# Kernel optimization log

Hardware: AMD Instinct MI355X
Metric: run time of the kernel (lower is better)

The kernel has to match this reference:

```python
import jax, jax.numpy as jnp
import numpy as np

B, S, I, H = 64, 1024, 512, 512


def setup_inputs() -> dict:
    key = jax.random.key(0)
    ks = jax.random.split(key, 6)
    stdv = 1.0 / np.sqrt(H)
    return {
        "inputs": jax.random.normal(ks[0], (B, S, I), dtype=jnp.float32),
        "h0": jax.random.normal(ks[1], (1, B, H), dtype=jnp.float32),
        "weight_ih": jax.random.uniform(ks[2], (H, I), jnp.float32, -stdv, stdv),
        "weight_hh": jax.random.uniform(ks[3], (H, H), jnp.float32, -stdv, stdv),
        "bias_ih": jax.random.uniform(ks[4], (H,), jnp.float32, -stdv, stdv),
        "bias_hh": jax.random.uniform(ks[5], (H,), jnp.float32, -stdv, stdv),
    }


def reference(inputs, h0, weight_ih, weight_hh, bias_ih, bias_hh):
    batch = inputs.shape[0]
    hidd = bias_hh.shape[0]
    # Precompute the input projection for all timesteps in one big GEMM:
    # [B, S, I] @ [I, H] -> [B, S, H], plus both biases.
    x_proj = jnp.einsum("bsi,hi->bsh", inputs, weight_ih) + bias_ih + bias_hh
    h_init = h0.reshape(batch, hidd)

    def step(h_prev, xp_t):  # xp_t: [B, H]
        h_t = jax.nn.relu(xp_t + h_prev @ weight_hh.T)
        return h_t, h_t

    h_final, outs = jax.lax.scan(step, h_init, jnp.swapaxes(x_proj, 0, 1))
    outputs = jnp.swapaxes(outs, 0, 1)  # [B, S, H]
    return outputs, h_final[None, :, :]
```

## Files before the change

kernel.cpp:

```cpp
#include <hip/hip_runtime.h>

#define B_ 64
#define S_ 1024
#define I_ 512
#define H_ 512
#define SH_ (S_ * H_)
#define OUT_H (B_ * SH_)
#define BH_ (B_ * H_)

__global__ __launch_bounds__(256) void xproj_kernel(
    const float* __restrict__ A, const float* __restrict__ W,
    const float* __restrict__ bih, const float* __restrict__ bhh,
    float* __restrict__ out)
{
  __shared__ float As[16][132];
  __shared__ float Bs[16][132];
  const int tid = threadIdx.x;
  const int m0 = blockIdx.x * 128;
  const int n0 = blockIdx.y * 128;

  float acc[8][8];
  #pragma unroll
  for (int i = 0; i < 8; ++i)
    #pragma unroll
    for (int j = 0; j < 8; ++j) acc[i][j] = 0.f;

  const int mb = (tid >> 4) * 8;
  const int nb = (tid & 15) * 8;

  for (int kb = 0; kb < I_ / 16; ++kb) {
    const int k0 = kb * 16;
    __syncthreads();
    #pragma unroll
    for (int l = 0; l < 2; ++l) {
      int s  = tid + l * 256;
      int ml = s >> 2;
      int kc = s & 3;
      float4 av = *(const float4*)(A + (size_t)(m0 + ml) * I_ + k0 + kc * 4);
      As[kc*4+0][ml] = av.x; As[kc*4+1][ml] = av.y;
      As[kc*4+2][ml] = av.z; As[kc*4+3][ml] = av.w;
      float4 bv = *(const float4*)(W + (size_t)(n0 + ml) * I_ + k0 + kc * 4);
      Bs[kc*4+0][ml] = bv.x; Bs[kc*4+1][ml] = bv.y;
      Bs[kc*4+2][ml] = bv.z; Bs[kc*4+3][ml] = bv.w;
    }
    __syncthreads();
    #pragma unroll
    for (int k = 0; k < 16; ++k) {
      float4 a0 = *(const float4*)&As[k][mb];
      float4 a1 = *(const float4*)&As[k][mb + 4];
      float4 b0 = *(const float4*)&Bs[k][nb];
      float4 b1 = *(const float4*)&Bs[k][nb + 4];
      float a[8] = {a0.x,a0.y,a0.z,a0.w,a1.x,a1.y,a1.z,a1.w};
      float b[8] = {b0.x,b0.y,b0.z,b0.w,b1.x,b1.y,b1.z,b1.w};
      #pragma unroll
      for (int i = 0; i < 8; ++i)
        #pragma unroll
        for (int j = 0; j < 8; ++j) acc[i][j] += a[i] * b[j];
    }
  }

  float bias[8];
  #pragma unroll
  for (int j = 0; j < 8; ++j) bias[j] = bih[n0 + nb + j] + bhh[n0 + nb + j];
  #pragma unroll
  for (int i = 0; i < 8; ++i) {
    float4 v0 = make_float4(acc[i][0]+bias[0], acc[i][1]+bias[1],
                            acc[i][2]+bias[2], acc[i][3]+bias[3]);
    float4 v1 = make_float4(acc[i][4]+bias[4], acc[i][5]+bias[5],
                            acc[i][6]+bias[6], acc[i][7]+bias[7]);
    float* o = out + (size_t)(m0 + mb + i) * H_ + n0 + nb;
    *(float4*)o       = v0;
    *(float4*)(o + 4) = v1;
  }
}

__global__ __launch_bounds__(256) void init_kernel(unsigned* __restrict__ hbu)
{
  int i = blockIdx.x * 256 + threadIdx.x;
  if (i < BH_) hbu[i] = 0u;
}

#define FMA4(A, W4, s) \
  A.x += W4.x * (s); A.y += W4.y * (s); A.z += W4.z * (s); A.w += W4.w * (s)
#define FMA16(A, hA, hB, hC, hD) \
  FMA4(A, w00, hA.x); FMA4(A, w01, hA.y); FMA4(A, w02, hA.z); FMA4(A, w03, hA.w); \
  FMA4(A, w04, hB.x); FMA4(A, w05, hB.y); FMA4(A, w06, hB.z); FMA4(A, w07, hB.w); \
  FMA4(A, w08, hC.x); FMA4(A, w09, hC.y); FMA4(A, w10, hC.z); FMA4(A, w11, hC.w); \
  FMA4(A, w12, hD.x); FMA4(A, w13, hD.y); FMA4(A, w14, hD.z); FMA4(A, w15, hD.w)

__global__ __launch_bounds__(512)
__attribute__((amdgpu_waves_per_eu(2, 2)))
void recur_kernel(
    const float* __restrict__ Whh, const float* __restrict__ h0,
    float* __restrict__ out, unsigned* __restrict__ hbu)
{
  const int tid   = threadIdx.x;
  const int bg    = blockIdx.x & 31;
  const int ns    = blockIdx.x >> 5;
  const int b0    = bg * 2;
  const int obase = ns * 64;
  const int o4    = tid & 15;
  const int kq    = tid >> 4;
  const int w     = tid >> 6;
  const int lane  = tid & 63;
  const int ep    = w & 1;

  __shared__ float hsh[2 * H_];
  __shared__ float red[32][132];

  const float* wp = Whh + (size_t)(obase + o4 * 4) * H_ + kq * 16;
  float4 r0a = *(const float4*)(wp            );
  float4 r0b = *(const float4*)(wp         + 4);
  float4 r0c = *(const float4*)(wp         + 8);
  float4 r0d = *(const float4*)(wp        + 12);
  float4 r1a = *(const float4*)(wp +   H_     );
  float4 r1b = *(const float4*)(wp +   H_ + 4);
  float4 r1c = *(const float4*)(wp +   H_ + 8);
  float4 r1d = *(const float4*)(wp +   H_ +12);
  float4 r2a = *(const float4*)(wp + 2*H_     );
  float4 r2b = *(const float4*)(wp + 2*H_ + 4);
  float4 r2c = *(const float4*)(wp + 2*H_ + 8);
  float4 r2d = *(const float4*)(wp + 2*H_ +12);
  float4 r3a = *(const float4*)(wp + 3*H_     );
  float4 r3b = *(const float4*)(wp + 3*H_ + 4);
  float4 r3c = *(const float4*)(wp + 3*H_ + 8);
  float4 r3d = *(const float4*)(wp + 3*H_ +12);
  float4 w00 = make_float4(r0a.x, r1a.x, r2a.x, r3a.x);
  float4 w01 = make_float4(r0a.y, r1a.y, r2a.y, r3a.y);
  float4 w02 = make_float4(r0a.z, r1a.z, r2a.z, r3a.z);
  float4 w03 = make_float4(r0a.w, r1a.w, r2a.w, r3a.w);
  float4 w04 = make_float4(r0b.x, r1b.x, r2b.x, r3b.x);
  float4 w05 = make_float4(r0b.y, r1b.y, r2b.y, r3b.y);
  float4 w06 = make_float4(r0b.z, r1b.z, r2b.z, r3b.z);
  float4 w07 = make_float4(r0b.w, r1b.w, r2b.w, r3b.w);
  float4 w08 = make_float4(r0c.x, r1c.x, r2c.x, r3c.x);
  float4 w09 = make_float4(r0c.y, r1c.y, r2c.y, r3c.y);
  float4 w10 = make_float4(r0c.z, r1c.z, r2c.z, r3c.z);
  float4 w11 = make_float4(r0c.w, r1c.w, r2c.w, r3c.w);
  float4 w12 = make_float4(r0d.x, r1d.x, r2d.x, r3d.x);
  float4 w13 = make_float4(r0d.y, r1d.y, r2d.y, r3d.y);
  float4 w14 = make_float4(r0d.z, r1d.z, r2d.z, r3d.z);
  float4 w15 = make_float4(r0d.w, r1d.w, r2d.w, r3d.w);

  float* outp = out + (size_t)(b0 + ep) * SH_ + obase + lane;
  unsigned* hdb = hbu + (size_t)(b0 + ep) * H_ + obase + lane;

  for (int t = 0; t < S_; ++t) {
    const bool fin = ((w >> 1) == (t & 3));

    float xp = 0.f;
    if (fin) xp = *outp;

    if (t == 0) {
      const float* hp = h0 + b0 * H_;
      hsh[tid]       = hp[tid];
      hsh[tid + 512] = hp[tid + 512];
    } else {
      const unsigned* hs = hbu + (t & 1) * BH_ + b0 * H_;
      const unsigned expct = ((unsigned)t >> 1) & 1u;
      unsigned a0 = __hip_atomic_load(hs + tid,       __ATOMIC_RELAXED,
                                      __HIP_MEMORY_SCOPE_AGENT);
      unsigned a1 = __hip_atomic_load(hs + tid + 512, __ATOMIC_RELAXED,
                                      __HIP_MEMORY_SCOPE_AGENT);
      while ((a0 >> 31) != expct) {
        __builtin_amdgcn_s_sleep(1);
        a0 = __hip_atomic_load(hs + tid, __ATOMIC_RELAXED,
                               __HIP_MEMORY_SCOPE_AGENT);
      }
      while ((a1 >> 31) != expct) {
        __builtin_amdgcn_s_sleep(1);
        a1 = __hip_atomic_load(hs + tid + 512, __ATOMIC_RELAXED,
                               __HIP_MEMORY_SCOPE_AGENT);
      }
      hsh[tid]       = __uint_as_float(a0 & 0x7fffffffu);
      hsh[tid + 512] = __uint_as_float(a1 & 0x7fffffffu);
    }
    __syncthreads();

    const float* hp0 = hsh + kq * 16;
    float4 hA = *(const float4*)(hp0     );
    float4 hB = *(const float4*)(hp0 +  4);
    float4 hC = *(const float4*)(hp0 +  8);
    float4 hD = *(const float4*)(hp0 + 12);
    float4 aA = make_float4(0.f, 0.f, 0.f, 0.f);
    FMA16(aA, hA, hB, hC, hD);

    const float* hp1 = hsh + H_ + kq * 16;
    float4 hE = *(const float4*)(hp1     );
    float4 hF = *(const float4*)(hp1 +  4);
    float4 hG = *(const float4*)(hp1 +  8);
    float4 hH = *(const float4*)(hp1 + 12);
    float4 aB = make_float4(0.f, 0.f, 0.f, 0.f);
    FMA16(aB, hE, hF, hG, hH);

    *(float4*)&red[kq][o4 * 4]      = aA;
    *(float4*)&red[kq][64 + o4 * 4] = aB;
    __syncthreads();

    if (fin) {
      const int idx = ep * 64 + lane;
      float s0 = 0.f, s1 = 0.f, s2 = 0.f, s3 = 0.f;
      #pragma unroll
      for (int q = 0; q < 32; q += 4) {
        s0 += red[q    ][idx];
        s1 += red[q + 1][idx];
        s2 += red[q + 2][idx];
        s3 += red[q + 3][idx];
      }
      float pre = xp + ((s0 + s1) + (s2 + s3));
      float v = pre > 0.f ? pre : 0.f;
      const unsigned tg = ((((unsigned)(t + 1)) >> 1) & 1u) << 31;
      __hip_atomic_store(hdb + ((t + 1) & 1) * BH_,
                         (__float_as_uint(v) & 0x7fffffffu) | tg,
                         __ATOMIC_RELAXED, __HIP_MEMORY_SCOPE_AGENT);
      *outp = v;
      if (t == S_ - 1)
        out[(size_t)OUT_H + (size_t)(b0 + ep) * H_ + obase + lane] = v;
    }
    outp += H_;
  }
}

extern "C" void kernel_launch(void* const* d_in, const int* in_sizes, int n_in,
                              void* d_out, int out_size, void* d_ws, size_t ws_size,
                              hipStream_t stream)
{
  const float* inputs = (const float*)d_in[0];
  const float* h0     = (const float*)d_in[1];
  const float* w_ih   = (const float*)d_in[2];
  const float* w_hh   = (const float*)d_in[3];
  const float* b_ih   = (const float*)d_in[4];
  const float* b_hh   = (const float*)d_in[5];
  float* out = (float*)d_out;

  unsigned* hbu = (unsigned*)d_ws;

  dim3 g1(512, 4);
  xproj_kernel<<<g1, 256, 0, stream>>>(inputs, w_ih, b_ih, b_hh, out);
  init_kernel<<<128, 256, 0, stream>>>(hbu);
  recur_kernel<<<256, 512, 0, stream>>>(w_hh, h0, out, hbu);
}
```

Measured before the change: 2.177 ms.

## Remove per-step barrier via per-wave private h staging and double-buffered reduction

Each wave now loads exactly the 64-wide slice of h it needs for both batch rows into its own shared buffer. It then waits only on its own LDS writes instead of a block-wide __syncthreads, which removes one barrier per timestep. The reduction buffer is double-buffered by timestep parity so the one remaining barrier is enough to avoid write-after-read hazards. The spin-wait loops also drop s_sleep to cut polling latency, at the cost of more memory traffic while spinning.

```diff
diff --git a/kernel.cpp b/kernel.cpp
--- a/kernel.cpp
+++ b/kernel.cpp
@@ -103,10 +103,11 @@
   const int kq    = tid >> 4;
   const int w     = tid >> 6;
   const int lane  = tid & 63;
+  const int kql   = (lane >> 4);
   const int ep    = w & 1;
 
-  __shared__ float hsh[2 * H_];
-  __shared__ float red[32][132];
+  __shared__ float hshw[8][128];
+  __shared__ float red[2][32][132];
 
   const float* wp = Whh + (size_t)(obase + o4 * 4) * H_ + kq * 16;
   float4 r0a = *(const float4*)(wp            );
@@ -145,39 +146,41 @@
   float* outp = out + (size_t)(b0 + ep) * SH_ + obase + lane;
   unsigned* hdb = hbu + (size_t)(b0 + ep) * H_ + obase + lane;
 
+  const int ksl = w * 64 + lane;
+
   for (int t = 0; t < S_; ++t) {
     const bool fin = ((w >> 1) == (t & 3));
 
     float xp = 0.f;
     if (fin) xp = *outp;
 
+    float v0, v1;
     if (t == 0) {
-      const float* hp = h0 + b0 * H_;
-      hsh[tid]       = hp[tid];
-      hsh[tid + 512] = hp[tid + 512];
+      const float* hp = h0 + (size_t)b0 * H_ + ksl;
+      v0 = hp[0];
+      v1 = hp[H_];
     } else {
-      const unsigned* hs = hbu + (t & 1) * BH_ + b0 * H_;
+      const unsigned* hs = hbu + (t & 1) * BH_ + (size_t)b0 * H_ + ksl;
       const unsigned expct = ((unsigned)t >> 1) & 1u;
-      unsigned a0 = __hip_atomic_load(hs + tid,       __ATOMIC_RELAXED,
+      unsigned a0 = __hip_atomic_load(hs,      __ATOMIC_RELAXED,
                                       __HIP_MEMORY_SCOPE_AGENT);
-      unsigned a1 = __hip_atomic_load(hs + tid + 512, __ATOMIC_RELAXED,
+      unsigned a1 = __hip_atomic_load(hs + H_, __ATOMIC_RELAXED,
                                       __HIP_MEMORY_SCOPE_AGENT);
-      while ((a0 >> 31) != expct) {
-        __builtin_amdgcn_s_sleep(1);
-        a0 = __hip_atomic_load(hs + tid, __ATOMIC_RELAXED,
+      while ((a0 >> 31) != expct)
+        a0 = __hip_atomic_load(hs,      __ATOMIC_RELAXED,
                                __HIP_MEMORY_SCOPE_AGENT);
-      }
-      while ((a1 >> 31) != expct) {
-        __builtin_amdgcn_s_sleep(1);
-        a1 = __hip_atomic_load(hs + tid + 512, __ATOMIC_RELAXED,
+      while ((a1 >> 31) != expct)
+        a1 = __hip_atomic_load(hs + H_, __ATOMIC_RELAXED,
                                __HIP_MEMORY_SCOPE_AGENT);
-      }
-      hsh[tid]       = __uint_as_float(a0 & 0x7fffffffu);
-      hsh[tid + 512] = __uint_as_float(a1 & 0x7fffffffu);
-    }
-    __syncthreads();
-
-    const float* hp0 = hsh + kq * 16;
+      v0 = __uint_as_float(a0 & 0x7fffffffu);
+      v1 = __uint_as_float(a1 & 0x7fffffffu);
+    }
+    hshw[w][lane]      = v0;
+    hshw[w][64 + lane] = v1;
+    asm volatile("s_waitcnt lgkmcnt(0)" ::: "memory");
+    __builtin_amdgcn_sched_barrier(0);
+
+    const float* hp0 = &hshw[w][kql * 16];
     float4 hA = *(const float4*)(hp0     );
     float4 hB = *(const float4*)(hp0 +  4);
     float4 hC = *(const float4*)(hp0 +  8);
@@ -185,7 +188,7 @@
     float4 aA = make_float4(0.f, 0.f, 0.f, 0.f);
     FMA16(aA, hA, hB, hC, hD);
 
-    const float* hp1 = hsh + H_ + kq * 16;
+    const float* hp1 = &hshw[w][64 + kql * 16];
     float4 hE = *(const float4*)(hp1     );
     float4 hF = *(const float4*)(hp1 +  4);
     float4 hG = *(const float4*)(hp1 +  8);
@@ -193,8 +196,9 @@
     float4 aB = make_float4(0.f, 0.f, 0.f, 0.f);
     FMA16(aB, hE, hF, hG, hH);
 
-    *(float4*)&red[kq][o4 * 4]      = aA;
-    *(float4*)&red[kq][64 + o4 * 4] = aB;
+    float (*rb)[132] = red[t & 1];
+    *(float4*)&rb[kq][o4 * 4]      = aA;
+    *(float4*)&rb[kq][64 + o4 * 4] = aB;
     __syncthreads();
 
     if (fin) {
@@ -202,10 +206,10 @@
       float s0 = 0.f, s1 = 0.f, s2 = 0.f, s3 = 0.f;
       #pragma unroll
       for (int q = 0; q < 32; q += 4) {
-        s0 += red[q    ][idx];
-        s1 += red[q + 1][idx];
-        s2 += red[q + 2][idx];
-        s3 += red[q + 3][idx];
+        s0 += rb[q    ][idx];
+        s1 += rb[q + 1][idx];
+        s2 += rb[q + 2][idx];
+        s3 += rb[q + 3][idx];
       }
       float pre = xp + ((s0 + s1) + (s2 + s3));
       float v = pre > 0.f ? pre : 0.f;
```

Measured after the change: 2.162 ms. No clear change (-0.7%).
